# Optimization experiments

Hardware: AMD Instinct MI355X
Metric: run time of the kernel (lower is better)

The kernel has to match this reference:

```python
import jax, jax.numpy as jnp
import numpy as np
import math

B, L, H, NH = 8, 512, 512, 8
DH = H // NH


def setup_inputs() -> dict:
    key = jax.random.key(0)
    ks = jax.random.split(key, 12)
    src = jax.random.normal(ks[0], (B, L, H), dtype=jnp.float32)
    seq_len = jax.random.randint(ks[1], (B,), L // 2, L + 1).astype(jnp.int32)
    seq_len = seq_len.at[0].set(L)  # guarantee max(seq_len) == L
    pe = jax.random.normal(ks[2], (2 * L, H), dtype=jnp.float32) * 0.02
    s = 1.0 / math.sqrt(H)
    Wq = jax.random.normal(ks[3], (H, H), dtype=jnp.float32) * s
    bq = jnp.zeros((H,), jnp.float32)
    Wk = jax.random.normal(ks[4], (H, H), dtype=jnp.float32) * s
    bk = jnp.zeros((H,), jnp.float32)
    Wv = jax.random.normal(ks[5], (H, H), dtype=jnp.float32) * s
    bv = jnp.zeros((H,), jnp.float32)
    Wr = jax.random.normal(ks[6], (H, H), dtype=jnp.float32) * s
    br = jnp.zeros((H,), jnp.float32)
    u = jax.random.normal(ks[7], (NH, DH), dtype=jnp.float32) * 0.02
    v = jax.random.normal(ks[8], (NH, DH), dtype=jnp.float32) * 0.02
    gamma = jnp.ones((H,), jnp.float32)
    beta = jnp.zeros((H,), jnp.float32)
    return dict(src=src, seq_len=seq_len, pe=pe, Wq=Wq, bq=bq, Wk=Wk, bk=bk,
                Wv=Wv, bv=bv, Wr=Wr, br=br, u=u, v=v, gamma=gamma, beta=beta)


def reference(src, seq_len, pe, Wq, bq, Wk, bk, Wv, bv, Wr, br, u, v, gamma, beta):
    b, l, h = src.shape
    dh = h // NH
    # relative distance rel[i,j] = j - i, lookup pe[rel + L]  -> [L, L, H]
    rel = jnp.arange(l)[None, :] - jnp.arange(l)[:, None]
    R = pe[rel + l]
    # projections (torch Linear: y = x W^T + b)
    q = src @ Wq.T + bq
    k = src @ Wk.T + bk
    val = src @ Wv.T + bv
    R = R @ Wr.T + br
    # split heads
    q = q.reshape(b, l, NH, dh)
    k = k.reshape(b, l, NH, dh)
    val = val.reshape(b, l, NH, dh)
    R = R.reshape(l, l, NH, dh)
    # Transformer-XL score terms
    A = jnp.einsum('bihd,bjhd->bhij', q, k)
    Bt = jnp.einsum('bihd,ijhd->bhij', q, R)
    C = jnp.einsum('hd,bjhd->bhj', u, k)[:, :, None, :]
    D = jnp.einsum('ijhd,hd->hij', R, v)[None]
    scores = (A + Bt + C + D) / math.sqrt(dh)
    # key-side padding mask
    mask = jnp.arange(l)[None, :] < seq_len[:, None]  # [B, L]
    scores = jnp.where(mask[:, None, None, :], scores, jnp.float32(-1e15))
    attn = jax.nn.softmax(scores, axis=-1)
    out = jnp.einsum('bhij,bjhd->bihd', attn, val).reshape(b, l, h)
    res = src + out
    # LayerNorm (eps=1e-5) then exact GELU
    mu = jnp.mean(res, axis=-1, keepdims=True)
    var = jnp.mean((res - mu) ** 2, axis=-1, keepdims=True)
    ln = (res - mu) * jax.lax.rsqrt(var + 1e-5) * gamma + beta
    return jax.nn.gelu(ln, approximate=False)
```

## Files before the change

### kernel.cpp

```cpp
#include <hip/hip_runtime.h>
#include <math.h>

#define Bn 8
#define Ln 512
#define Hn 512
#define NHn 8
#define DHn 64

typedef __attribute__((ext_vector_type(8))) short short8;
typedef __attribute__((ext_vector_type(4))) float f32x4;

__device__ __forceinline__ unsigned short f2bf(float f) {
    unsigned int u = __float_as_uint(f);
    unsigned int r = (u + 0x7FFFu + ((u >> 16) & 1u)) >> 16;
    return (unsigned short)r;
}
__device__ __forceinline__ float bf2f(unsigned short s) {
    return __uint_as_float(((unsigned int)s) << 16);
}

__global__ __launch_bounds__(256) void convert_kernel(
    const float* __restrict__ src, const float* __restrict__ pe,
    const float* __restrict__ Wq, const float* __restrict__ Wk,
    const float* __restrict__ Wv, const float* __restrict__ Wr,
    const float* __restrict__ bq, const float* __restrict__ bk,
    const float* __restrict__ bv,
    unsigned short* __restrict__ src_bf, unsigned short* __restrict__ pe_bf,
    unsigned short* __restrict__ Wcat_bf, unsigned short* __restrict__ Wr_bf,
    float* __restrict__ bcat)
{
    const int bid = blockIdx.x;
    const int tid = threadIdx.x;
    const float* in; unsigned short* outp; int base4;
    if (bid < 2048)      { in = src; outp = src_bf;           base4 = bid; }
    else if (bid < 2560) { in = pe;  outp = pe_bf;            base4 = bid - 2048; }
    else if (bid < 2816) { in = Wq;  outp = Wcat_bf;          base4 = bid - 2560; }
    else if (bid < 3072) { in = Wk;  outp = Wcat_bf + 262144; base4 = bid - 2816; }
    else if (bid < 3328) { in = Wv;  outp = Wcat_bf + 524288; base4 = bid - 3072; }
    else if (bid < 3584) { in = Wr;  outp = Wr_bf;            base4 = bid - 3328; }
    else {
        const int idx = (bid - 3584) * 256 + tid;
        if (idx < 512)            bcat[idx] = bq[idx];
        else if (idx < 1024)      bcat[idx] = bk[idx - 512];
        else if (idx < 1536)      bcat[idx] = bv[idx - 1024];
        return;
    }
    const int i4 = (base4 * 256 + tid) * 4;
    float4 x = *(const float4*)&in[i4];
    ushort4 o;
    o.x = f2bf(x.x); o.y = f2bf(x.y); o.z = f2bf(x.z); o.w = f2bf(x.w);
    *(ushort4*)&outp[i4] = o;
}

#define GSTR 72
__global__ __launch_bounds__(256) void gemm_kernel(
    const unsigned short* __restrict__ src_bf,
    const unsigned short* __restrict__ Wcat_bf,
    const unsigned short* __restrict__ pe_bf,
    const unsigned short* __restrict__ Wr_bf,
    const float* __restrict__ bcat, const float* __restrict__ br,
    unsigned short* __restrict__ QKb,
    unsigned short* __restrict__ VTg,
    unsigned short* __restrict__ Rpb)
{
    const int bid = blockIdx.x;
    int mode, m0, n0;
    const unsigned short *A, *B;
    if (bid < 256) {
        mode = 0; n0 = (bid & 7) * 128; m0 = (bid >> 3) * 128;
        A = src_bf + (size_t)m0 * 512;
        B = Wcat_bf + (size_t)n0 * 512;
    } else if (bid < 384) {
        mode = 1; m0 = ((bid - 256) & 3) * 128; n0 = ((bid - 256) >> 2) * 128;
        A = Wcat_bf + (size_t)(1024 + m0) * 512;
        B = src_bf + (size_t)n0 * 512;
    } else {
        mode = 2; n0 = ((bid - 384) & 3) * 128; m0 = ((bid - 384) >> 2) * 128;
        A = pe_bf + (size_t)m0 * 512;
        B = Wr_bf + (size_t)n0 * 512;
    }

    __shared__ unsigned short As[128 * GSTR];
    __shared__ unsigned short Bs[128 * GSTR];

    const int t = threadIdx.x;
    const int wave = t >> 6, lane = t & 63;
    const int wm = (wave >> 1) * 64;
    const int wn = (wave & 1) * 64;
    const int l = lane & 15, g = lane >> 4;

    f32x4 acc[4][4] = {};

    const int srow = wave * 32 + (lane >> 2);
    const int scol = (lane & 3) * 16;
    const unsigned short* Ag = A + (size_t)srow * 512 + scol;
    const unsigned short* Bg = B + (size_t)srow * 512 + scol;
    unsigned short* AsW = &As[srow * GSTR + scol];
    unsigned short* BsW = &Bs[srow * GSTR + scol];

    uint4 a0 = *(const uint4*)(Ag);
    uint4 a1 = *(const uint4*)(Ag + 8);
    uint4 a2 = *(const uint4*)(Ag + 16 * 512);
    uint4 a3 = *(const uint4*)(Ag + 16 * 512 + 8);
    uint4 b0 = *(const uint4*)(Bg);
    uint4 b1 = *(const uint4*)(Bg + 8);
    uint4 b2 = *(const uint4*)(Bg + 16 * 512);
    uint4 b3 = *(const uint4*)(Bg + 16 * 512 + 8);

    for (int k0 = 0; k0 < 512; k0 += 64) {
        __syncthreads();
        *(uint4*)(AsW)                = a0;
        *(uint4*)(AsW + 8)            = a1;
        *(uint4*)(AsW + 16 * GSTR)    = a2;
        *(uint4*)(AsW + 16 * GSTR + 8) = a3;
        *(uint4*)(BsW)                = b0;
        *(uint4*)(BsW + 8)            = b1;
        *(uint4*)(BsW + 16 * GSTR)    = b2;
        *(uint4*)(BsW + 16 * GSTR + 8) = b3;
        __syncthreads();

        if (k0 + 64 < 512) {
            const int kn = k0 + 64;
            a0 = *(const uint4*)(Ag + kn);
            a1 = *(const uint4*)(Ag + kn + 8);
            a2 = *(const uint4*)(Ag + kn + 16 * 512);
            a3 = *(const uint4*)(Ag + kn + 16 * 512 + 8);
            b0 = *(const uint4*)(Bg + kn);
            b1 = *(const uint4*)(Bg + kn + 8);
            b2 = *(const uint4*)(Bg + kn + 16 * 512);
            b3 = *(const uint4*)(Bg + kn + 16 * 512 + 8);
        }

        #pragma unroll
        for (int kk = 0; kk < 2; ++kk) {
            short8 af[4], bf[4];
            #pragma unroll
            for (int mt = 0; mt < 4; ++mt)
                af[mt] = *(const short8*)&As[(wm + mt * 16 + l) * GSTR + kk * 32 + g * 8];
            #pragma unroll
            for (int nt = 0; nt < 4; ++nt)
                bf[nt] = *(const short8*)&Bs[(wn + nt * 16 + l) * GSTR + kk * 32 + g * 8];
            #pragma unroll
            for (int mt = 0; mt < 4; ++mt)
                #pragma unroll
                for (int nt = 0; nt < 4; ++nt)
                    acc[mt][nt] = __builtin_amdgcn_mfma_f32_16x16x32_bf16(
                        af[mt], bf[nt], acc[mt][nt], 0, 0, 0);
        }
    }

    const int crow = g * 4;
    const int ccol = l;
    if (mode == 0) {
        #pragma unroll
        for (int mt = 0; mt < 4; ++mt)
            #pragma unroll
            for (int nt = 0; nt < 4; ++nt) {
                const int n = n0 + wn + nt * 16 + ccol;
                const float bn = bcat[n];
                #pragma unroll
                for (int r = 0; r < 4; ++r) {
                    const int m = m0 + wm + mt * 16 + crow + r;
                    QKb[(size_t)m * 1024 + n] = f2bf(acc[mt][nt][r] + bn);
                }
            }
    } else if (mode == 1) {
        #pragma unroll
        for (int mt = 0; mt < 4; ++mt)
            #pragma unroll
            for (int nt = 0; nt < 4; ++nt) {
                const int n = n0 + wn + nt * 16 + ccol;
                #pragma unroll
                for (int r = 0; r < 4; ++r) {
                    const int dv = m0 + wm + mt * 16 + crow + r;
                    VTg[(size_t)dv * 4096 + n] = f2bf(acc[mt][nt][r] + bcat[1024 + dv]);
                }
            }
    } else {
        #pragma unroll
        for (int mt = 0; mt < 4; ++mt)
            #pragma unroll
            for (int nt = 0; nt < 4; ++nt) {
                const int n = n0 + wn + nt * 16 + ccol;
                const float bn = br[n];
                #pragma unroll
                for (int r = 0; r < 4; ++r) {
                    const int m = m0 + wm + mt * 16 + crow + r;
                    Rpb[(size_t)m * 512 + n] = f2bf(acc[mt][nt][r] + bn);
                }
            }
    }
}

#define PADK 72
__global__ __launch_bounds__(256) void attn_kernel(
    const unsigned short* __restrict__ QKb,
    const unsigned short* __restrict__ VTg,
    const unsigned short* __restrict__ Rpb,
    const float* __restrict__ u, const float* __restrict__ v,
    const int* __restrict__ seq_len, unsigned short* __restrict__ Ob)
{
    const int i0 = blockIdx.x * 64;
    const int h  = blockIdx.y;
    const int b  = blockIdx.z;
    const int slen = seq_len[b];
    const int njt = (slen + 63) >> 6;

    __shared__ unsigned short k_s [64 * PADK];
    __shared__ unsigned short vT_s[64 * PADK];
    __shared__ unsigned short rs_s[64 * PADK];
    __shared__ unsigned short p_s [64 * PADK];
    __shared__ unsigned short qrTT[128 * 72];

    const int t = threadIdx.x;
    const int wave = t >> 6, lane = t & 63;
    const int l = lane & 15, g = lane >> 4;

    short8 af_qu[2], af_qv[2];
    {
        const unsigned short* qrow =
            QKb + (size_t)(b * 512 + i0 + wave * 16 + l) * 1024 + h * 64;
        #pragma unroll
        for (int kk = 0; kk < 2; ++kk) {
            const int c = kk * 32 + g * 8;
            unsigned short q8[8];
            *(uint4*)q8 = *(const uint4*)(qrow + c);
            float4 u0 = *(const float4*)(u + h * 64 + c);
            float4 u1 = *(const float4*)(u + h * 64 + c + 4);
            float4 v0 = *(const float4*)(v + h * 64 + c);
            float4 v1 = *(const float4*)(v + h * 64 + c + 4);
            float uf[8] = {u0.x,u0.y,u0.z,u0.w,u1.x,u1.y,u1.z,u1.w};
            float vf[8] = {v0.x,v0.y,v0.z,v0.w,v1.x,v1.y,v1.z,v1.w};
            short8 qu, qv;
            #pragma unroll
            for (int e = 0; e < 8; ++e) {
                float qf = bf2f(q8[e]);
                qu[e] = (short)f2bf(qf + uf[e]);
                qv[e] = (short)f2bf(qf + vf[e]);
            }
            af_qu[kk] = qu; af_qv[kk] = qv;
        }
    }

    float m_run[4], l_run[4];
    f32x4 accO[4] = {};
    #pragma unroll
    for (int r = 0; r < 4; ++r) { m_run[r] = -3.0e38f; l_run[r] = 0.f; }

    const int jr = t >> 2, c0 = (t & 3) * 16;

    auto btChunk = [&](int slot0) {
        #pragma unroll
        for (int nt8 = 0; nt8 < 4; ++nt8) {
            f32x4 a = {};
            #pragma unroll
            for (int kk = 0; kk < 2; ++kk) {
                short8 br8 = *(const short8*)&rs_s[(nt8 * 16 + l) * PADK + kk * 32 + g * 8];
                a = __builtin_amdgcn_mfma_f32_16x16x32_bf16(af_qv[kk], br8, a, 0, 0, 0);
            }
            const int sl = slot0 + nt8 * 16 + l;
            ushort4 w4;
            w4.x = f2bf(a[0]); w4.y = f2bf(a[1]); w4.z = f2bf(a[2]); w4.w = f2bf(a[3]);
            *(ushort4*)(qrTT + sl * 72 + wave * 16 + g * 4) = w4;
        }
    };

    const unsigned short* rpA = Rpb + (size_t)(448 - i0 + jr) * 512 + h * 64 + c0;
    uint4 rA0 = *(const uint4*)(rpA);
    uint4 rA1 = *(const uint4*)(rpA + 8);
    const unsigned short* kp0 = QKb + (size_t)(b * 512 + jr) * 1024 + 512 + h * 64 + c0;
    uint4 kc0 = *(const uint4*)(kp0), kc1 = *(const uint4*)(kp0 + 8);
    const unsigned short* vp0 = VTg + (size_t)(h * 64 + jr) * 4096 + b * 512 + c0;
    uint4 vc0 = *(const uint4*)(vp0), vc1 = *(const uint4*)(vp0 + 8);
    const unsigned short* rp0 = Rpb + (size_t)(512 - i0 + jr) * 512 + h * 64 + c0;
    uint4 rc0 = *(const uint4*)(rp0), rc1 = *(const uint4*)(rp0 + 8);

    *(uint4*)(rs_s + jr * PADK + c0)     = rA0;
    *(uint4*)(rs_s + jr * PADK + c0 + 8) = rA1;
    __syncthreads();
    btChunk((448 - i0) & 127);

    for (int jt = 0; jt < njt; ++jt) {
        const int j0 = jt * 64;
        __syncthreads();

        *(uint4*)(k_s  + jr * PADK + c0)     = kc0;
        *(uint4*)(k_s  + jr * PADK + c0 + 8) = kc1;
        *(uint4*)(vT_s + jr * PADK + c0)     = vc0;
        *(uint4*)(vT_s + jr * PADK + c0 + 8) = vc1;
        *(uint4*)(rs_s + jr * PADK + c0)     = rc0;
        *(uint4*)(rs_s + jr * PADK + c0 + 8) = rc1;
        __syncthreads();

        if (jt + 1 < njt) {
            const unsigned short* kp =
                QKb + (size_t)(b * 512 + j0 + 64 + jr) * 1024 + 512 + h * 64 + c0;
            kc0 = *(const uint4*)(kp); kc1 = *(const uint4*)(kp + 8);
            const unsigned short* vp =
                VTg + (size_t)(h * 64 + jr) * 4096 + b * 512 + j0 + 64 + c0;
            vc0 = *(const uint4*)(vp); vc1 = *(const uint4*)(vp + 8);
            const unsigned short* rp =
                Rpb + (size_t)(j0 + 64 - i0 + 512 + jr) * 512 + h * 64 + c0;
            rc0 = *(const uint4*)(rp); rc1 = *(const uint4*)(rp + 8);
        }

        btChunk((j0 - i0 + 512) & 127);

        f32x4 accA[4];
        #pragma unroll
        for (int nt = 0; nt < 4; ++nt) {
            f32x4 a = {};
            #pragma unroll
            for (int kk = 0; kk < 2; ++kk) {
                short8 bk8 = *(const short8*)&k_s[(nt * 16 + l) * PADK + kk * 32 + g * 8];
                a = __builtin_amdgcn_mfma_f32_16x16x32_bf16(af_qu[kk], bk8, a, 0, 0, 0);
            }
            accA[nt] = a;
        }

        float sv[4][4];
        #pragma unroll
        for (int nt = 0; nt < 4; ++nt)
            #pragma unroll
            for (int r = 0; r < 4; ++r) {
                const int il = wave * 16 + g * 4 + r;
                const int slot = (j0 + nt * 16 + l - i0 - il + 512) & 127;
                const float qr = bf2f(qrTT[slot * 72 + il]);
                float s = (accA[nt][r] + qr) * 0.125f;
                if (j0 + nt * 16 + l >= slen) s = -1e15f;
                sv[nt][r] = s;
            }

        float alpha_r[4];
        #pragma unroll
        for (int r = 0; r < 4; ++r) {
            float tm = fmaxf(fmaxf(sv[0][r], sv[1][r]), fmaxf(sv[2][r], sv[3][r]));
            tm = fmaxf(tm, __shfl_xor(tm, 1, 64));
            tm = fmaxf(tm, __shfl_xor(tm, 2, 64));
            tm = fmaxf(tm, __shfl_xor(tm, 4, 64));
            tm = fmaxf(tm, __shfl_xor(tm, 8, 64));
            const float mn = fmaxf(m_run[r], tm);
            alpha_r[r] = __expf(m_run[r] - mn);
            m_run[r] = mn;
            float ss = 0.f;
            #pragma unroll
            for (int nt = 0; nt < 4; ++nt) {
                const float pe_ = __expf(sv[nt][r] - mn);
                sv[nt][r] = pe_; ss += pe_;
            }
            ss += __shfl_xor(ss, 1, 64);
            ss += __shfl_xor(ss, 2, 64);
            ss += __shfl_xor(ss, 4, 64);
            ss += __shfl_xor(ss, 8, 64);
            l_run[r] = l_run[r] * alpha_r[r] + ss;
        }

        #pragma unroll
        for (int nt = 0; nt < 4; ++nt)
            #pragma unroll
            for (int r = 0; r < 4; ++r)
                p_s[(wave * 16 + g * 4 + r) * PADK + nt * 16 + l] = f2bf(sv[nt][r]);

        #pragma unroll
        for (int nt = 0; nt < 4; ++nt)
            #pragma unroll
            for (int r = 0; r < 4; ++r)
                accO[nt][r] *= alpha_r[r];

        short8 pa[2];
        #pragma unroll
        for (int kk = 0; kk < 2; ++kk)
            pa[kk] = *(const short8*)&p_s[(wave * 16 + l) * PADK + kk * 32 + g * 8];
        #pragma unroll
        for (int nt = 0; nt < 4; ++nt) {
            #pragma unroll
            for (int kk = 0; kk < 2; ++kk) {
                short8 bv8 = *(const short8*)&vT_s[(nt * 16 + l) * PADK + kk * 32 + g * 8];
                accO[nt] = __builtin_amdgcn_mfma_f32_16x16x32_bf16(pa[kk], bv8, accO[nt], 0, 0, 0);
            }
        }
    }

    float inv[4];
    #pragma unroll
    for (int r = 0; r < 4; ++r) inv[r] = 1.0f / l_run[r];
    #pragma unroll
    for (int nt = 0; nt < 4; ++nt)
        #pragma unroll
        for (int r = 0; r < 4; ++r)
            Ob[(size_t)(b * 512 + i0 + wave * 16 + g * 4 + r) * 512 + h * 64 + nt * 16 + l]
                = f2bf(accO[nt][r] * inv[r]);
}

__global__ __launch_bounds__(256) void ln_gelu_kernel(
    const float* __restrict__ src, const unsigned short* __restrict__ Ob,
    const float* __restrict__ gamma, const float* __restrict__ beta,
    float* __restrict__ out)
{
    const int row  = blockIdx.x * 4 + (threadIdx.x >> 6);
    const int lane = threadIdx.x & 63;
    const int c0   = lane * 8;
    const float* s = &src[(size_t)row * 512 + c0];
    float4 s0 = *(const float4*)(s);
    float4 s1 = *(const float4*)(s + 4);
    unsigned short o8[8];
    *(uint4*)o8 = *(const uint4*)(Ob + (size_t)row * 512 + c0);
    float x[8];
    x[0] = s0.x + bf2f(o8[0]); x[1] = s0.y + bf2f(o8[1]);
    x[2] = s0.z + bf2f(o8[2]); x[3] = s0.w + bf2f(o8[3]);
    x[4] = s1.x + bf2f(o8[4]); x[5] = s1.y + bf2f(o8[5]);
    x[6] = s1.z + bf2f(o8[6]); x[7] = s1.w + bf2f(o8[7]);
    float sum = 0.f;
    #pragma unroll
    for (int e = 0; e < 8; ++e) sum += x[e];
    #pragma unroll
    for (int off = 32; off >= 1; off >>= 1) sum += __shfl_xor(sum, off, 64);
    const float mean = sum * (1.0f / 512.0f);
    float var = 0.f;
    #pragma unroll
    for (int e = 0; e < 8; ++e) { float d = x[e] - mean; var += d * d; }
    #pragma unroll
    for (int off = 32; off >= 1; off >>= 1) var += __shfl_xor(var, off, 64);
    var *= (1.0f / 512.0f);
    const float inv = rsqrtf(var + 1e-5f);
    float4 g0 = *(const float4*)(gamma + c0);
    float4 g1 = *(const float4*)(gamma + c0 + 4);
    float4 b0 = *(const float4*)(beta + c0);
    float4 b1 = *(const float4*)(beta + c0 + 4);
    float gm[8] = {g0.x,g0.y,g0.z,g0.w,g1.x,g1.y,g1.z,g1.w};
    float bt[8] = {b0.x,b0.y,b0.z,b0.w,b1.x,b1.y,b1.z,b1.w};
    float r8[8];
    #pragma unroll
    for (int e = 0; e < 8; ++e) {
        float ln = (x[e] - mean) * inv * gm[e] + bt[e];
        r8[e] = 0.5f * ln * (1.0f + erff(ln * 0.70710678118654752f));
    }
    float* op = &out[(size_t)row * 512 + c0];
    *(float4*)(op)     = make_float4(r8[0], r8[1], r8[2], r8[3]);
    *(float4*)(op + 4) = make_float4(r8[4], r8[5], r8[6], r8[7]);
}

extern "C" void kernel_launch(void* const* d_in, const int* in_sizes, int n_in,
                              void* d_out, int out_size, void* d_ws, size_t ws_size,
                              hipStream_t stream)
{
    const float* src     = (const float*)d_in[0];
    const int*   seq_len = (const int*)  d_in[1];
    const float* pe      = (const float*)d_in[2];
    const float* Wq      = (const float*)d_in[3];
    const float* bq      = (const float*)d_in[4];
    const float* Wk      = (const float*)d_in[5];
    const float* bk      = (const float*)d_in[6];
    const float* Wv      = (const float*)d_in[7];
    const float* bv      = (const float*)d_in[8];
    const float* Wr      = (const float*)d_in[9];
    const float* br      = (const float*)d_in[10];
    const float* u       = (const float*)d_in[11];
    const float* v       = (const float*)d_in[12];
    const float* gamma   = (const float*)d_in[13];
    const float* beta    = (const float*)d_in[14];
    float* out = (float*)d_out;

    char* w = (char*)d_ws;
    unsigned short* QKb     = (unsigned short*)(w);
    unsigned short* VTg     = (unsigned short*)(w + 8388608);
    unsigned short* Rpb     = (unsigned short*)(w + 12582912);
    unsigned short* Ob      = (unsigned short*)(w + 13631488);
    unsigned short* src_bf  = (unsigned short*)(w + 17825792);
    unsigned short* pe_bf   = (unsigned short*)(w + 22020096);
    unsigned short* Wcat_bf = (unsigned short*)(w + 23068672);
    unsigned short* Wr_bf   = (unsigned short*)(w + 24641536);
    float*          bcat    = (float*)         (w + 25165824);

    convert_kernel<<<dim3(3590), 256, 0, stream>>>(
        src, pe, Wq, Wk, Wv, Wr, bq, bk, bv,
        src_bf, pe_bf, Wcat_bf, Wr_bf, bcat);

    gemm_kernel<<<dim3(416), 256, 0, stream>>>(
        src_bf, Wcat_bf, pe_bf, Wr_bf, bcat, br, QKb, VTg, Rpb);

    attn_kernel<<<dim3(8, NHn, Bn), 256, 0, stream>>>(QKb, VTg, Rpb, u, v, seq_len, Ob);

    ln_gelu_kernel<<<dim3(Bn * Ln / 4), 256, 0, stream>>>(src, Ob, gamma, beta, out);
}
```

Measured before the change: 133.6 us.

## Load attention K/V/R operands directly from global and compute row sums via MFMA

The attention kernel no longer stages K, V^T and relative-position tiles through shared memory with register prefetch and two block barriers per tile. Each wave now reads its MFMA B-operands straight from global memory, so only the per-wave qrTT ring and P buffers remain in LDS. The softmax denominator is also accumulated by an extra MFMA of P against a ones vector, replacing the cross-lane shuffle reduction. This removes barriers and LDS traffic, but each of the four waves re-fetches the same K/V/R rows from global memory. It also loses the explicit prefetch that hid load latency.

Measured after the change: 171.7 us. +28.5%, slower.

```diff
diff --git a/kernel.cpp b/kernel.cpp
--- a/kernel.cpp
+++ b/kernel.cpp
@@ -192,7 +192,7 @@
     }
 }
 
-#define PADK 72
+#define PADQ 72
 __global__ __launch_bounds__(256) void attn_kernel(
     const unsigned short* __restrict__ QKb,
     const unsigned short* __restrict__ VTg,
@@ -206,11 +206,8 @@
     const int slen = seq_len[b];
     const int njt = (slen + 63) >> 6;
 
-    __shared__ unsigned short k_s [64 * PADK];
-    __shared__ unsigned short vT_s[64 * PADK];
-    __shared__ unsigned short rs_s[64 * PADK];
-    __shared__ unsigned short p_s [64 * PADK];
-    __shared__ unsigned short qrTT[128 * 72];
+    __shared__ unsigned short qrTT[128 * PADQ];
+    __shared__ unsigned short p_s [64 * PADQ];
 
     const int t = threadIdx.x;
     const int wave = t >> 6, lane = t & 63;
@@ -242,77 +239,50 @@
         }
     }
 
-    float m_run[4], l_run[4];
+    short8 ones8;
+    #pragma unroll
+    for (int e = 0; e < 8; ++e) ones8[e] = (short)0x3F80;
+
+    float m_run[4];
+    #pragma unroll
+    for (int r = 0; r < 4; ++r) m_run[r] = -3.0e38f;
     f32x4 accO[4] = {};
-    #pragma unroll
-    for (int r = 0; r < 4; ++r) { m_run[r] = -3.0e38f; l_run[r] = 0.f; }
-
-    const int jr = t >> 2, c0 = (t & 3) * 16;
-
-    auto btChunk = [&](int slot0) {
+    f32x4 accL = {};
+
+    auto btChunk = [&](int rowBase) {
         #pragma unroll
         for (int nt8 = 0; nt8 < 4; ++nt8) {
+            const unsigned short* rrow =
+                Rpb + (size_t)(rowBase + nt8 * 16 + l) * 512 + h * 64;
             f32x4 a = {};
             #pragma unroll
             for (int kk = 0; kk < 2; ++kk) {
-                short8 br8 = *(const short8*)&rs_s[(nt8 * 16 + l) * PADK + kk * 32 + g * 8];
+                short8 br8 = *(const short8*)(rrow + kk * 32 + g * 8);
                 a = __builtin_amdgcn_mfma_f32_16x16x32_bf16(af_qv[kk], br8, a, 0, 0, 0);
             }
-            const int sl = slot0 + nt8 * 16 + l;
+            const int sl = (rowBase & 127) + nt8 * 16 + l;
             ushort4 w4;
             w4.x = f2bf(a[0]); w4.y = f2bf(a[1]); w4.z = f2bf(a[2]); w4.w = f2bf(a[3]);
-            *(ushort4*)(qrTT + sl * 72 + wave * 16 + g * 4) = w4;
+            *(ushort4*)(qrTT + sl * PADQ + wave * 16 + g * 4) = w4;
         }
     };
 
-    const unsigned short* rpA = Rpb + (size_t)(448 - i0 + jr) * 512 + h * 64 + c0;
-    uint4 rA0 = *(const uint4*)(rpA);
-    uint4 rA1 = *(const uint4*)(rpA + 8);
-    const unsigned short* kp0 = QKb + (size_t)(b * 512 + jr) * 1024 + 512 + h * 64 + c0;
-    uint4 kc0 = *(const uint4*)(kp0), kc1 = *(const uint4*)(kp0 + 8);
-    const unsigned short* vp0 = VTg + (size_t)(h * 64 + jr) * 4096 + b * 512 + c0;
-    uint4 vc0 = *(const uint4*)(vp0), vc1 = *(const uint4*)(vp0 + 8);
-    const unsigned short* rp0 = Rpb + (size_t)(512 - i0 + jr) * 512 + h * 64 + c0;
-    uint4 rc0 = *(const uint4*)(rp0), rc1 = *(const uint4*)(rp0 + 8);
-
-    *(uint4*)(rs_s + jr * PADK + c0)     = rA0;
-    *(uint4*)(rs_s + jr * PADK + c0 + 8) = rA1;
-    __syncthreads();
-    btChunk((448 - i0) & 127);
+    btChunk(448 - i0);
 
     for (int jt = 0; jt < njt; ++jt) {
         const int j0 = jt * 64;
-        __syncthreads();
-
-        *(uint4*)(k_s  + jr * PADK + c0)     = kc0;
-        *(uint4*)(k_s  + jr * PADK + c0 + 8) = kc1;
-        *(uint4*)(vT_s + jr * PADK + c0)     = vc0;
-        *(uint4*)(vT_s + jr * PADK + c0 + 8) = vc1;
-        *(uint4*)(rs_s + jr * PADK + c0)     = rc0;
-        *(uint4*)(rs_s + jr * PADK + c0 + 8) = rc1;
-        __syncthreads();
-
-        if (jt + 1 < njt) {
-            const unsigned short* kp =
-                QKb + (size_t)(b * 512 + j0 + 64 + jr) * 1024 + 512 + h * 64 + c0;
-            kc0 = *(const uint4*)(kp); kc1 = *(const uint4*)(kp + 8);
-            const unsigned short* vp =
-                VTg + (size_t)(h * 64 + jr) * 4096 + b * 512 + j0 + 64 + c0;
-            vc0 = *(const uint4*)(vp); vc1 = *(const uint4*)(vp + 8);
-            const unsigned short* rp =
-                Rpb + (size_t)(j0 + 64 - i0 + 512 + jr) * 512 + h * 64 + c0;
-            rc0 = *(const uint4*)(rp); rc1 = *(const uint4*)(rp + 8);
-        }
-
-        btChunk((j0 - i0 + 512) & 127);
+
+        btChunk(j0 + 512 - i0);
 
         f32x4 accA[4];
         #pragma unroll
         for (int nt = 0; nt < 4; ++nt) {
+            const unsigned short* krow =
+                QKb + (size_t)(b * 512 + j0 + nt * 16 + l) * 1024 + 512 + h * 64;
             f32x4 a = {};
             #pragma unroll
             for (int kk = 0; kk < 2; ++kk) {
-                short8 bk8 = *(const short8*)&k_s[(nt * 16 + l) * PADK + kk * 32 + g * 8];
+                short8 bk8 = *(const short8*)(krow + kk * 32 + g * 8);
                 a = __builtin_amdgcn_mfma_f32_16x16x32_bf16(af_qu[kk], bk8, a, 0, 0, 0);
             }
             accA[nt] = a;
@@ -320,16 +290,17 @@
 
         float sv[4][4];
         #pragma unroll
-        for (int nt = 0; nt < 4; ++nt)
+        for (int nt = 0; nt < 4; ++nt) {
+            const bool masked = (j0 + nt * 16 + l) >= slen;
             #pragma unroll
             for (int r = 0; r < 4; ++r) {
                 const int il = wave * 16 + g * 4 + r;
                 const int slot = (j0 + nt * 16 + l - i0 - il + 512) & 127;
-                const float qr = bf2f(qrTT[slot * 72 + il]);
+                const float qr = bf2f(qrTT[slot * PADQ + il]);
                 float s = (accA[nt][r] + qr) * 0.125f;
-                if (j0 + nt * 16 + l >= slen) s = -1e15f;
-                sv[nt][r] = s;
-            }
+                sv[nt][r] = masked ? -1e15f : s;
+            }
+        }
 
         float alpha_r[4];
         #pragma unroll
@@ -342,40 +313,41 @@
             const float mn = fmaxf(m_run[r], tm);
             alpha_r[r] = __expf(m_run[r] - mn);
             m_run[r] = mn;
-            float ss = 0.f;
-            #pragma unroll
-            for (int nt = 0; nt < 4; ++nt) {
-                const float pe_ = __expf(sv[nt][r] - mn);
-                sv[nt][r] = pe_; ss += pe_;
-            }
-            ss += __shfl_xor(ss, 1, 64);
-            ss += __shfl_xor(ss, 2, 64);
-            ss += __shfl_xor(ss, 4, 64);
-            ss += __shfl_xor(ss, 8, 64);
-            l_run[r] = l_run[r] * alpha_r[r] + ss;
+            #pragma unroll
+            for (int nt = 0; nt < 4; ++nt)
+                sv[nt][r] = __expf(sv[nt][r] - mn);
         }
 
         #pragma unroll
         for (int nt = 0; nt < 4; ++nt)
             #pragma unroll
             for (int r = 0; r < 4; ++r)
-                p_s[(wave * 16 + g * 4 + r) * PADK + nt * 16 + l] = f2bf(sv[nt][r]);
+                p_s[(wave * 16 + g * 4 + r) * PADQ + nt * 16 + l] = f2bf(sv[nt][r]);
 
         #pragma unroll
         for (int nt = 0; nt < 4; ++nt)
             #pragma unroll
             for (int r = 0; r < 4; ++r)
                 accO[nt][r] *= alpha_r[r];
+        #pragma unroll
+        for (int r = 0; r < 4; ++r) accL[r] *= alpha_r[r];
 
         short8 pa[2];
         #pragma unroll
         for (int kk = 0; kk < 2; ++kk)
-            pa[kk] = *(const short8*)&p_s[(wave * 16 + l) * PADK + kk * 32 + g * 8];
+            pa[kk] = *(const short8*)&p_s[(wave * 16 + l) * PADQ + kk * 32 + g * 8];
+
+        #pragma unroll
+        for (int kk = 0; kk < 2; ++kk)
+            accL = __builtin_amdgcn_mfma_f32_16x16x32_bf16(pa[kk], ones8, accL, 0, 0, 0);
+
         #pragma unroll
         for (int nt = 0; nt < 4; ++nt) {
+            const unsigned short* vrow =
+                VTg + (size_t)(h * 64 + nt * 16 + l) * 4096 + b * 512 + j0;
             #pragma unroll
             for (int kk = 0; kk < 2; ++kk) {
-                short8 bv8 = *(const short8*)&vT_s[(nt * 16 + l) * PADK + kk * 32 + g * 8];
+                short8 bv8 = *(const short8*)(vrow + kk * 32 + g * 8);
                 accO[nt] = __builtin_amdgcn_mfma_f32_16x16x32_bf16(pa[kk], bv8, accO[nt], 0, 0, 0);
             }
         }
@@ -383,7 +355,7 @@
 
     float inv[4];
     #pragma unroll
-    for (int r = 0; r < 4; ++r) inv[r] = 1.0f / l_run[r];
+    for (int r = 0; r < 4; ++r) inv[r] = 1.0f / accL[r];
     #pragma unroll
     for (int nt = 0; nt < 4; ++nt)
         #pragma unroll
```

## Fuse fp32-to-bf16 conversion into GEMM loads; compute softmax row sums via MFMA

Applied to the files above, without the earlier changes.

Removes the separate conversion kernel. The GEMM now reads the fp32 inputs and weights directly and packs them to bf16 while staging into shared memory, which drops one launch and an extra round trip through the workspace. The GEMM's global reads double in size and its register use rises. In attention, the per-row softmax denominator is now accumulated with an MFMA against a vector of ones instead of shuffle reductions. That sum is taken from the bf16-rounded probabilities, which slightly changes numerics.

Result: slower. 139.0 us (+4.1%).

```diff
diff --git a/kernel.cpp b/kernel.cpp
--- a/kernel.cpp
+++ b/kernel.cpp
@@ -18,66 +18,36 @@
 __device__ __forceinline__ float bf2f(unsigned short s) {
     return __uint_as_float(((unsigned int)s) << 16);
 }
-
-__global__ __launch_bounds__(256) void convert_kernel(
-    const float* __restrict__ src, const float* __restrict__ pe,
-    const float* __restrict__ Wq, const float* __restrict__ Wk,
-    const float* __restrict__ Wv, const float* __restrict__ Wr,
-    const float* __restrict__ bq, const float* __restrict__ bk,
-    const float* __restrict__ bv,
-    unsigned short* __restrict__ src_bf, unsigned short* __restrict__ pe_bf,
-    unsigned short* __restrict__ Wcat_bf, unsigned short* __restrict__ Wr_bf,
-    float* __restrict__ bcat)
-{
-    const int bid = blockIdx.x;
-    const int tid = threadIdx.x;
-    const float* in; unsigned short* outp; int base4;
-    if (bid < 2048)      { in = src; outp = src_bf;           base4 = bid; }
-    else if (bid < 2560) { in = pe;  outp = pe_bf;            base4 = bid - 2048; }
-    else if (bid < 2816) { in = Wq;  outp = Wcat_bf;          base4 = bid - 2560; }
-    else if (bid < 3072) { in = Wk;  outp = Wcat_bf + 262144; base4 = bid - 2816; }
-    else if (bid < 3328) { in = Wv;  outp = Wcat_bf + 524288; base4 = bid - 3072; }
-    else if (bid < 3584) { in = Wr;  outp = Wr_bf;            base4 = bid - 3328; }
-    else {
-        const int idx = (bid - 3584) * 256 + tid;
-        if (idx < 512)            bcat[idx] = bq[idx];
-        else if (idx < 1024)      bcat[idx] = bk[idx - 512];
-        else if (idx < 1536)      bcat[idx] = bv[idx - 1024];
-        return;
-    }
-    const int i4 = (base4 * 256 + tid) * 4;
-    float4 x = *(const float4*)&in[i4];
-    ushort4 o;
-    o.x = f2bf(x.x); o.y = f2bf(x.y); o.z = f2bf(x.z); o.w = f2bf(x.w);
-    *(ushort4*)&outp[i4] = o;
+__device__ __forceinline__ unsigned int pk2(float lo, float hi) {
+    return (unsigned int)f2bf(lo) | ((unsigned int)f2bf(hi) << 16);
 }
 
 #define GSTR 72
 __global__ __launch_bounds__(256) void gemm_kernel(
-    const unsigned short* __restrict__ src_bf,
-    const unsigned short* __restrict__ Wcat_bf,
-    const unsigned short* __restrict__ pe_bf,
-    const unsigned short* __restrict__ Wr_bf,
-    const float* __restrict__ bcat, const float* __restrict__ br,
+    const float* __restrict__ src, const float* __restrict__ Wq,
+    const float* __restrict__ Wk,  const float* __restrict__ Wv,
+    const float* __restrict__ pe,  const float* __restrict__ Wr,
+    const float* __restrict__ bq,  const float* __restrict__ bk,
+    const float* __restrict__ bv,  const float* __restrict__ br,
     unsigned short* __restrict__ QKb,
     unsigned short* __restrict__ VTg,
     unsigned short* __restrict__ Rpb)
 {
     const int bid = blockIdx.x;
     int mode, m0, n0;
-    const unsigned short *A, *B;
+    const float *A, *B;
     if (bid < 256) {
         mode = 0; n0 = (bid & 7) * 128; m0 = (bid >> 3) * 128;
-        A = src_bf + (size_t)m0 * 512;
-        B = Wcat_bf + (size_t)n0 * 512;
+        A = src + (size_t)m0 * 512;
+        B = (n0 < 512) ? (Wq + (size_t)n0 * 512) : (Wk + (size_t)(n0 - 512) * 512);
     } else if (bid < 384) {
         mode = 1; m0 = ((bid - 256) & 3) * 128; n0 = ((bid - 256) >> 2) * 128;
-        A = Wcat_bf + (size_t)(1024 + m0) * 512;
-        B = src_bf + (size_t)n0 * 512;
+        A = Wv + (size_t)m0 * 512;
+        B = src + (size_t)n0 * 512;
     } else {
         mode = 2; n0 = ((bid - 384) & 3) * 128; m0 = ((bid - 384) >> 2) * 128;
-        A = pe_bf + (size_t)m0 * 512;
-        B = Wr_bf + (size_t)n0 * 512;
+        A = pe + (size_t)m0 * 512;
+        B = Wr + (size_t)n0 * 512;
     }
 
     __shared__ unsigned short As[128 * GSTR];
@@ -93,42 +63,62 @@
 
     const int srow = wave * 32 + (lane >> 2);
     const int scol = (lane & 3) * 16;
-    const unsigned short* Ag = A + (size_t)srow * 512 + scol;
-    const unsigned short* Bg = B + (size_t)srow * 512 + scol;
+    const float* Ag = A + (size_t)srow * 512 + scol;
+    const float* Bg = B + (size_t)srow * 512 + scol;
     unsigned short* AsW = &As[srow * GSTR + scol];
     unsigned short* BsW = &Bs[srow * GSTR + scol];
 
-    uint4 a0 = *(const uint4*)(Ag);
-    uint4 a1 = *(const uint4*)(Ag + 8);
-    uint4 a2 = *(const uint4*)(Ag + 16 * 512);
-    uint4 a3 = *(const uint4*)(Ag + 16 * 512 + 8);
-    uint4 b0 = *(const uint4*)(Bg);
-    uint4 b1 = *(const uint4*)(Bg + 8);
-    uint4 b2 = *(const uint4*)(Bg + 16 * 512);
-    uint4 b3 = *(const uint4*)(Bg + 16 * 512 + 8);
+    float4 a[8], b[8];
+    a[0] = *(const float4*)(Ag);            a[1] = *(const float4*)(Ag + 4);
+    a[2] = *(const float4*)(Ag + 8);        a[3] = *(const float4*)(Ag + 12);
+    a[4] = *(const float4*)(Ag + 16 * 512);      a[5] = *(const float4*)(Ag + 16 * 512 + 4);
+    a[6] = *(const float4*)(Ag + 16 * 512 + 8);  a[7] = *(const float4*)(Ag + 16 * 512 + 12);
+    b[0] = *(const float4*)(Bg);            b[1] = *(const float4*)(Bg + 4);
+    b[2] = *(const float4*)(Bg + 8);        b[3] = *(const float4*)(Bg + 12);
+    b[4] = *(const float4*)(Bg + 16 * 512);      b[5] = *(const float4*)(Bg + 16 * 512 + 4);
+    b[6] = *(const float4*)(Bg + 16 * 512 + 8);  b[7] = *(const float4*)(Bg + 16 * 512 + 12);
 
     for (int k0 = 0; k0 < 512; k0 += 64) {
         __syncthreads();
-        *(uint4*)(AsW)                = a0;
-        *(uint4*)(AsW + 8)            = a1;
-        *(uint4*)(AsW + 16 * GSTR)    = a2;
-        *(uint4*)(AsW + 16 * GSTR + 8) = a3;
-        *(uint4*)(BsW)                = b0;
-        *(uint4*)(BsW + 8)            = b1;
-        *(uint4*)(BsW + 16 * GSTR)    = b2;
-        *(uint4*)(BsW + 16 * GSTR + 8) = b3;
+        {
+            uint4 w;
+            w.x = pk2(a[0].x, a[0].y); w.y = pk2(a[0].z, a[0].w);
+            w.z = pk2(a[1].x, a[1].y); w.w = pk2(a[1].z, a[1].w);
+            *(uint4*)(AsW) = w;
+            w.x = pk2(a[2].x, a[2].y); w.y = pk2(a[2].z, a[2].w);
+            w.z = pk2(a[3].x, a[3].y); w.w = pk2(a[3].z, a[3].w);
+            *(uint4*)(AsW + 8) = w;
+            w.x = pk2(a[4].x, a[4].y); w.y = pk2(a[4].z, a[4].w);
+            w.z = pk2(a[5].x, a[5].y); w.w = pk2(a[5].z, a[5].w);
+            *(uint4*)(AsW + 16 * GSTR) = w;
+            w.x = pk2(a[6].x, a[6].y); w.y = pk2(a[6].z, a[6].w);
+            w.z = pk2(a[7].x, a[7].y); w.w = pk2(a[7].z, a[7].w);
+            *(uint4*)(AsW + 16 * GSTR + 8) = w;
+            w.x = pk2(b[0].x, b[0].y); w.y = pk2(b[0].z, b[0].w);
+            w.z = pk2(b[1].x, b[1].y); w.w = pk2(b[1].z, b[1].w);
+            *(uint4*)(BsW) = w;
+            w.x = pk2(b[2].x, b[2].y); w.y = pk2(b[2].z, b[2].w);
+            w.z = pk2(b[3].x, b[3].y); w.w = pk2(b[3].z, b[3].w);
+            *(uint4*)(BsW + 8) = w;
+            w.x = pk2(b[4].x, b[4].y); w.y = pk2(b[4].z, b[4].w);
+            w.z = pk2(b[5].x, b[5].y); w.w = pk2(b[5].z, b[5].w);
+            *(uint4*)(BsW + 16 * GSTR) = w;
+            w.x = pk2(b[6].x, b[6].y); w.y = pk2(b[6].z, b[6].w);
+            w.z = pk2(b[7].x, b[7].y); w.w = pk2(b[7].z, b[7].w);
+            *(uint4*)(BsW + 16 * GSTR + 8) = w;
+        }
         __syncthreads();
 
         if (k0 + 64 < 512) {
             const int kn = k0 + 64;
-            a0 = *(const uint4*)(Ag + kn);
-            a1 = *(const uint4*)(Ag + kn + 8);
-            a2 = *(const uint4*)(Ag + kn + 16 * 512);
-            a3 = *(const uint4*)(Ag + kn + 16 * 512 + 8);
-            b0 = *(const uint4*)(Bg + kn);
-            b1 = *(const uint4*)(Bg + kn + 8);
-            b2 = *(const uint4*)(Bg + kn + 16 * 512);
-            b3 = *(const uint4*)(Bg + kn + 16 * 512 + 8);
+            a[0] = *(const float4*)(Ag + kn);            a[1] = *(const float4*)(Ag + kn + 4);
+            a[2] = *(const float4*)(Ag + kn + 8);        a[3] = *(const float4*)(Ag + kn + 12);
+            a[4] = *(const float4*)(Ag + kn + 16 * 512);      a[5] = *(const float4*)(Ag + kn + 16 * 512 + 4);
+            a[6] = *(const float4*)(Ag + kn + 16 * 512 + 8);  a[7] = *(const float4*)(Ag + kn + 16 * 512 + 12);
+            b[0] = *(const float4*)(Bg + kn);            b[1] = *(const float4*)(Bg + kn + 4);
+            b[2] = *(const float4*)(Bg + kn + 8);        b[3] = *(const float4*)(Bg + kn + 12);
+            b[4] = *(const float4*)(Bg + kn + 16 * 512);      b[5] = *(const float4*)(Bg + kn + 16 * 512 + 4);
+            b[6] = *(const float4*)(Bg + kn + 16 * 512 + 8);  b[7] = *(const float4*)(Bg + kn + 16 * 512 + 12);
         }
 
         #pragma unroll
@@ -152,12 +142,14 @@
     const int crow = g * 4;
     const int ccol = l;
     if (mode == 0) {
+        const float* bp0; int nofs;
+        if (n0 < 512) { bp0 = bq; nofs = 0; } else { bp0 = bk; nofs = 512; }
         #pragma unroll
         for (int mt = 0; mt < 4; ++mt)
             #pragma unroll
             for (int nt = 0; nt < 4; ++nt) {
                 const int n = n0 + wn + nt * 16 + ccol;
-                const float bn = bcat[n];
+                const float bn = bp0[n - nofs];
                 #pragma unroll
                 for (int r = 0; r < 4; ++r) {
                     const int m = m0 + wm + mt * 16 + crow + r;
@@ -173,7 +165,7 @@
                 #pragma unroll
                 for (int r = 0; r < 4; ++r) {
                     const int dv = m0 + wm + mt * 16 + crow + r;
-                    VTg[(size_t)dv * 4096 + n] = f2bf(acc[mt][nt][r] + bcat[1024 + dv]);
+                    VTg[(size_t)dv * 4096 + n] = f2bf(acc[mt][nt][r] + bv[dv]);
                 }
             }
     } else {
@@ -242,10 +234,15 @@
         }
     }
 
-    float m_run[4], l_run[4];
+    short8 ones8;
+    #pragma unroll
+    for (int e = 0; e < 8; ++e) ones8[e] = (short)0x3F80;
+
+    float m_run[4];
+    #pragma unroll
+    for (int r = 0; r < 4; ++r) m_run[r] = -3.0e38f;
     f32x4 accO[4] = {};
-    #pragma unroll
-    for (int r = 0; r < 4; ++r) { m_run[r] = -3.0e38f; l_run[r] = 0.f; }
+    f32x4 accL = {};
 
     const int jr = t >> 2, c0 = (t & 3) * 16;
 
@@ -320,16 +317,17 @@
 
         float sv[4][4];
         #pragma unroll
-        for (int nt = 0; nt < 4; ++nt)
+        for (int nt = 0; nt < 4; ++nt) {
+            const bool masked = (j0 + nt * 16 + l) >= slen;
             #pragma unroll
             for (int r = 0; r < 4; ++r) {
                 const int il = wave * 16 + g * 4 + r;
                 const int slot = (j0 + nt * 16 + l - i0 - il + 512) & 127;
                 const float qr = bf2f(qrTT[slot * 72 + il]);
                 float s = (accA[nt][r] + qr) * 0.125f;
-                if (j0 + nt * 16 + l >= slen) s = -1e15f;
-                sv[nt][r] = s;
-            }
+                sv[nt][r] = masked ? -1e15f : s;
+            }
+        }
 
         float alpha_r[4];
         #pragma unroll
@@ -342,17 +340,9 @@
             const float mn = fmaxf(m_run[r], tm);
             alpha_r[r] = __expf(m_run[r] - mn);
             m_run[r] = mn;
-            float ss = 0.f;
-            #pragma unroll
-            for (int nt = 0; nt < 4; ++nt) {
-                const float pe_ = __expf(sv[nt][r] - mn);
-                sv[nt][r] = pe_; ss += pe_;
-            }
-            ss += __shfl_xor(ss, 1, 64);
-            ss += __shfl_xor(ss, 2, 64);
-            ss += __shfl_xor(ss, 4, 64);
-            ss += __shfl_xor(ss, 8, 64);
-            l_run[r] = l_run[r] * alpha_r[r] + ss;
+            #pragma unroll
+            for (int nt = 0; nt < 4; ++nt)
+                sv[nt][r] = __expf(sv[nt][r] - mn);
         }
 
         #pragma unroll
@@ -366,11 +356,18 @@
             #pragma unroll
             for (int r = 0; r < 4; ++r)
                 accO[nt][r] *= alpha_r[r];
+        #pragma unroll
+        for (int r = 0; r < 4; ++r) accL[r] *= alpha_r[r];
 
         short8 pa[2];
         #pragma unroll
         for (int kk = 0; kk < 2; ++kk)
             pa[kk] = *(const short8*)&p_s[(wave * 16 + l) * PADK + kk * 32 + g * 8];
+
+        #pragma unroll
+        for (int kk = 0; kk < 2; ++kk)
+            accL = __builtin_amdgcn_mfma_f32_16x16x32_bf16(pa[kk], ones8, accL, 0, 0, 0);
+
         #pragma unroll
         for (int nt = 0; nt < 4; ++nt) {
             #pragma unroll
@@ -383,7 +380,7 @@
 
     float inv[4];
     #pragma unroll
-    for (int r = 0; r < 4; ++r) inv[r] = 1.0f / l_run[r];
+    for (int r = 0; r < 4; ++r) inv[r] = 1.0f / accL[r];
     #pragma unroll
     for (int nt = 0; nt < 4; ++nt)
         #pragma unroll
@@ -462,22 +459,13 @@
     float* out = (float*)d_out;
 
     char* w = (char*)d_ws;
-    unsigned short* QKb     = (unsigned short*)(w);
-    unsigned short* VTg     = (unsigned short*)(w + 8388608);
-    unsigned short* Rpb     = (unsigned short*)(w + 12582912);
-    unsigned short* Ob      = (unsigned short*)(w + 13631488);
-    unsigned short* src_bf  = (unsigned short*)(w + 17825792);
-    unsigned short* pe_bf   = (unsigned short*)(w + 22020096);
-    unsigned short* Wcat_bf = (unsigned short*)(w + 23068672);
-    unsigned short* Wr_bf   = (unsigned short*)(w + 24641536);
-    float*          bcat    = (float*)         (w + 25165824);
-
-    convert_kernel<<<dim3(3590), 256, 0, stream>>>(
-        src, pe, Wq, Wk, Wv, Wr, bq, bk, bv,
-        src_bf, pe_bf, Wcat_bf, Wr_bf, bcat);
+    unsigned short* QKb = (unsigned short*)(w);
+    unsigned short* VTg = (unsigned short*)(w + 8388608);
+    unsigned short* Rpb = (unsigned short*)(w + 12582912);
+    unsigned short* Ob  = (unsigned short*)(w + 13631488);
 
     gemm_kernel<<<dim3(416), 256, 0, stream>>>(
-        src_bf, Wcat_bf, pe_bf, Wr_bf, bcat, br, QKb, VTg, Rpb);
+        src, Wq, Wk, Wv, pe, Wr, bq, bk, bv, br, QKb, VTg, Rpb);
 
     attn_kernel<<<dim3(8, NHn, Bn), 256, 0, stream>>>(QKb, VTg, Rpb, u, v, seq_len, Ob);
 
```

## Halve GEMM M-tile for more blocks; compute softmax row sums via MFMA

Applied to the files above, without the earlier changes.

The projection GEMM tile shrinks from 128x128 to 64x128, doubling the grid to 832 blocks so more of the GPU's compute units are kept busy. The cost is less operand reuse per block and more redundant B-tile loads. In the attention kernel, the per-row softmax denominator is no longer a shuffle-reduction of the exp values. It is accumulated with an extra MFMA of the bf16 probability tile against a ones vector, which removes the xor-shuffle reductions but sums bf16-rounded probabilities. The mask test is also hoisted out of the inner loop.

Result: no change. 135.5 us (+1.5%).

```diff
diff --git a/kernel.cpp b/kernel.cpp
--- a/kernel.cpp
+++ b/kernel.cpp
@@ -66,33 +66,35 @@
     const int bid = blockIdx.x;
     int mode, m0, n0;
     const unsigned short *A, *B;
-    if (bid < 256) {
-        mode = 0; n0 = (bid & 7) * 128; m0 = (bid >> 3) * 128;
+    if (bid < 512) {
+        mode = 0; m0 = (bid >> 3) * 64; n0 = (bid & 7) * 128;
         A = src_bf + (size_t)m0 * 512;
         B = Wcat_bf + (size_t)n0 * 512;
-    } else if (bid < 384) {
-        mode = 1; m0 = ((bid - 256) & 3) * 128; n0 = ((bid - 256) >> 2) * 128;
+    } else if (bid < 768) {
+        const int idx = bid - 512;
+        mode = 1; m0 = (idx & 7) * 64; n0 = (idx >> 3) * 128;
         A = Wcat_bf + (size_t)(1024 + m0) * 512;
         B = src_bf + (size_t)n0 * 512;
     } else {
-        mode = 2; n0 = ((bid - 384) & 3) * 128; m0 = ((bid - 384) >> 2) * 128;
+        const int idx = bid - 768;
+        mode = 2; m0 = (idx >> 2) * 64; n0 = (idx & 3) * 128;
         A = pe_bf + (size_t)m0 * 512;
         B = Wr_bf + (size_t)n0 * 512;
     }
 
-    __shared__ unsigned short As[128 * GSTR];
+    __shared__ unsigned short As[64 * GSTR];
     __shared__ unsigned short Bs[128 * GSTR];
 
     const int t = threadIdx.x;
     const int wave = t >> 6, lane = t & 63;
-    const int wm = (wave >> 1) * 64;
+    const int wm = (wave >> 1) * 32;
     const int wn = (wave & 1) * 64;
     const int l = lane & 15, g = lane >> 4;
 
-    f32x4 acc[4][4] = {};
-
-    const int srow = wave * 32 + (lane >> 2);
-    const int scol = (lane & 3) * 16;
+    f32x4 acc[2][4] = {};
+
+    const int srow = t >> 2;
+    const int scol = (t & 3) * 16;
     const unsigned short* Ag = A + (size_t)srow * 512 + scol;
     const unsigned short* Bg = B + (size_t)srow * 512 + scol;
     unsigned short* AsW = &As[srow * GSTR + scol];
@@ -100,48 +102,42 @@
 
     uint4 a0 = *(const uint4*)(Ag);
     uint4 a1 = *(const uint4*)(Ag + 8);
-    uint4 a2 = *(const uint4*)(Ag + 16 * 512);
-    uint4 a3 = *(const uint4*)(Ag + 16 * 512 + 8);
     uint4 b0 = *(const uint4*)(Bg);
     uint4 b1 = *(const uint4*)(Bg + 8);
-    uint4 b2 = *(const uint4*)(Bg + 16 * 512);
-    uint4 b3 = *(const uint4*)(Bg + 16 * 512 + 8);
+    uint4 b2 = *(const uint4*)(Bg + 64 * 512);
+    uint4 b3 = *(const uint4*)(Bg + 64 * 512 + 8);
 
     for (int k0 = 0; k0 < 512; k0 += 64) {
         __syncthreads();
-        *(uint4*)(AsW)                = a0;
-        *(uint4*)(AsW + 8)            = a1;
-        *(uint4*)(AsW + 16 * GSTR)    = a2;
-        *(uint4*)(AsW + 16 * GSTR + 8) = a3;
-        *(uint4*)(BsW)                = b0;
-        *(uint4*)(BsW + 8)            = b1;
-        *(uint4*)(BsW + 16 * GSTR)    = b2;
-        *(uint4*)(BsW + 16 * GSTR + 8) = b3;
+        *(uint4*)(AsW)                 = a0;
+        *(uint4*)(AsW + 8)             = a1;
+        *(uint4*)(BsW)                 = b0;
+        *(uint4*)(BsW + 8)             = b1;
+        *(uint4*)(BsW + 64 * GSTR)     = b2;
+        *(uint4*)(BsW + 64 * GSTR + 8) = b3;
         __syncthreads();
 
         if (k0 + 64 < 512) {
             const int kn = k0 + 64;
             a0 = *(const uint4*)(Ag + kn);
             a1 = *(const uint4*)(Ag + kn + 8);
-            a2 = *(const uint4*)(Ag + kn + 16 * 512);
-            a3 = *(const uint4*)(Ag + kn + 16 * 512 + 8);
             b0 = *(const uint4*)(Bg + kn);
             b1 = *(const uint4*)(Bg + kn + 8);
-            b2 = *(const uint4*)(Bg + kn + 16 * 512);
-            b3 = *(const uint4*)(Bg + kn + 16 * 512 + 8);
+            b2 = *(const uint4*)(Bg + kn + 64 * 512);
+            b3 = *(const uint4*)(Bg + kn + 64 * 512 + 8);
         }
 
         #pragma unroll
         for (int kk = 0; kk < 2; ++kk) {
-            short8 af[4], bf[4];
-            #pragma unroll
-            for (int mt = 0; mt < 4; ++mt)
+            short8 af[2], bf[4];
+            #pragma unroll
+            for (int mt = 0; mt < 2; ++mt)
                 af[mt] = *(const short8*)&As[(wm + mt * 16 + l) * GSTR + kk * 32 + g * 8];
             #pragma unroll
             for (int nt = 0; nt < 4; ++nt)
                 bf[nt] = *(const short8*)&Bs[(wn + nt * 16 + l) * GSTR + kk * 32 + g * 8];
             #pragma unroll
-            for (int mt = 0; mt < 4; ++mt)
+            for (int mt = 0; mt < 2; ++mt)
                 #pragma unroll
                 for (int nt = 0; nt < 4; ++nt)
                     acc[mt][nt] = __builtin_amdgcn_mfma_f32_16x16x32_bf16(
@@ -153,7 +149,7 @@
     const int ccol = l;
     if (mode == 0) {
         #pragma unroll
-        for (int mt = 0; mt < 4; ++mt)
+        for (int mt = 0; mt < 2; ++mt)
             #pragma unroll
             for (int nt = 0; nt < 4; ++nt) {
                 const int n = n0 + wn + nt * 16 + ccol;
@@ -166,7 +162,7 @@
             }
     } else if (mode == 1) {
         #pragma unroll
-        for (int mt = 0; mt < 4; ++mt)
+        for (int mt = 0; mt < 2; ++mt)
             #pragma unroll
             for (int nt = 0; nt < 4; ++nt) {
                 const int n = n0 + wn + nt * 16 + ccol;
@@ -178,7 +174,7 @@
             }
     } else {
         #pragma unroll
-        for (int mt = 0; mt < 4; ++mt)
+        for (int mt = 0; mt < 2; ++mt)
             #pragma unroll
             for (int nt = 0; nt < 4; ++nt) {
                 const int n = n0 + wn + nt * 16 + ccol;
@@ -242,10 +238,15 @@
         }
     }
 
-    float m_run[4], l_run[4];
+    short8 ones8;
+    #pragma unroll
+    for (int e = 0; e < 8; ++e) ones8[e] = (short)0x3F80;
+
+    float m_run[4];
+    #pragma unroll
+    for (int r = 0; r < 4; ++r) m_run[r] = -3.0e38f;
     f32x4 accO[4] = {};
-    #pragma unroll
-    for (int r = 0; r < 4; ++r) { m_run[r] = -3.0e38f; l_run[r] = 0.f; }
+    f32x4 accL = {};
 
     const int jr = t >> 2, c0 = (t & 3) * 16;
 
@@ -320,16 +321,17 @@
 
         float sv[4][4];
         #pragma unroll
-        for (int nt = 0; nt < 4; ++nt)
+        for (int nt = 0; nt < 4; ++nt) {
+            const bool masked = (j0 + nt * 16 + l) >= slen;
             #pragma unroll
             for (int r = 0; r < 4; ++r) {
                 const int il = wave * 16 + g * 4 + r;
                 const int slot = (j0 + nt * 16 + l - i0 - il + 512) & 127;
                 const float qr = bf2f(qrTT[slot * 72 + il]);
                 float s = (accA[nt][r] + qr) * 0.125f;
-                if (j0 + nt * 16 + l >= slen) s = -1e15f;
-                sv[nt][r] = s;
-            }
+                sv[nt][r] = masked ? -1e15f : s;
+            }
+        }
 
         float alpha_r[4];
         #pragma unroll
@@ -342,17 +344,9 @@
             const float mn = fmaxf(m_run[r], tm);
             alpha_r[r] = __expf(m_run[r] - mn);
             m_run[r] = mn;
-            float ss = 0.f;
-            #pragma unroll
-            for (int nt = 0; nt < 4; ++nt) {
-                const float pe_ = __expf(sv[nt][r] - mn);
-                sv[nt][r] = pe_; ss += pe_;
-            }
-            ss += __shfl_xor(ss, 1, 64);
-            ss += __shfl_xor(ss, 2, 64);
-            ss += __shfl_xor(ss, 4, 64);
-            ss += __shfl_xor(ss, 8, 64);
-            l_run[r] = l_run[r] * alpha_r[r] + ss;
+            #pragma unroll
+            for (int nt = 0; nt < 4; ++nt)
+                sv[nt][r] = __expf(sv[nt][r] - mn);
         }
 
         #pragma unroll
@@ -366,11 +360,18 @@
             #pragma unroll
             for (int r = 0; r < 4; ++r)
                 accO[nt][r] *= alpha_r[r];
+        #pragma unroll
+        for (int r = 0; r < 4; ++r) accL[r] *= alpha_r[r];
 
         short8 pa[2];
         #pragma unroll
         for (int kk = 0; kk < 2; ++kk)
             pa[kk] = *(const short8*)&p_s[(wave * 16 + l) * PADK + kk * 32 + g * 8];
+
+        #pragma unroll
+        for (int kk = 0; kk < 2; ++kk)
+            accL = __builtin_amdgcn_mfma_f32_16x16x32_bf16(pa[kk], ones8, accL, 0, 0, 0);
+
         #pragma unroll
         for (int nt = 0; nt < 4; ++nt) {
             #pragma unroll
@@ -383,7 +384,7 @@
 
     float inv[4];
     #pragma unroll
-    for (int r = 0; r < 4; ++r) inv[r] = 1.0f / l_run[r];
+    for (int r = 0; r < 4; ++r) inv[r] = 1.0f / accL[r];
     #pragma unroll
     for (int nt = 0; nt < 4; ++nt)
         #pragma unroll
@@ -476,7 +477,7 @@
         src, pe, Wq, Wk, Wv, Wr, bq, bk, bv,
         src_bf, pe_bf, Wcat_bf, Wr_bf, bcat);
 
-    gemm_kernel<<<dim3(416), 256, 0, stream>>>(
+    gemm_kernel<<<dim3(832), 256, 0, stream>>>(
         src_bf, Wcat_bf, pe_bf, Wr_bf, bcat, br, QKb, VTg, Rpb);
 
     attn_kernel<<<dim3(8, NHn, Bn), 256, 0, stream>>>(QKb, VTg, Rpb, u, v, seq_len, Ob);
```
